# Optimization experiments

Measured on AMD Instinct MI355X. Metric: run time of the kernel, lower is better.

## Reference

```python
import jax, jax.numpy as jnp
import numpy as np

B, C, H, W = 4, 512, 64, 64
CQ = C // 8


def setup_inputs() -> dict:
    key = jax.random.key(0)
    ks = jax.random.split(key, 8)
    s_in = 1.0 / np.sqrt(C)
    return {
        "x": jax.random.normal(ks[0], (B, C, H, W), jnp.float32),
        "wq": jax.random.normal(ks[1], (CQ, C), jnp.float32) * s_in,
        "bq": jax.random.normal(ks[2], (CQ,), jnp.float32) * 0.01,
        "wk": jax.random.normal(ks[3], (CQ, C), jnp.float32) * s_in,
        "bk": jax.random.normal(ks[4], (CQ,), jnp.float32) * 0.01,
        "wv": jax.random.normal(ks[5], (C, C), jnp.float32) * s_in,
        "bv": jax.random.normal(ks[6], (C,), jnp.float32) * 0.01,
        "gamma": jax.random.normal(ks[7], (1,), jnp.float32) * 0.1,
    }


def reference(x, wq, bq, wk, bk, wv, bv, gamma):
    b, c, h, w = x.shape
    n = h * w
    xf = x.reshape(b, c, n)  # [B, C, N]; 1x1 conv == channel matmul
    q = jnp.einsum("oc,bcn->bon", wq, xf) + bq[None, :, None]  # [B, CQ, N]
    k = jnp.einsum("oc,bcn->bon", wk, xf) + bk[None, :, None]  # [B, CQ, N]
    v = jnp.einsum("oc,bcn->bon", wv, xf) + bv[None, :, None]  # [B, C, N]
    energy = jnp.einsum("bcn,bcm->bnm", q, k)  # [B, N, N]
    attn = jax.nn.softmax(energy, axis=-1)
    out = jnp.einsum("bcm,bnm->bcn", v, attn)  # [B, C, N]
    out = out.reshape(b, c, h, w)
    return gamma[0] * out + x
```

## Files before the change

kernel.cpp:

```cpp
#include <hip/hip_runtime.h>
#include <hip/hip_bf16.h>

#define BATCH 4
#define CH    512
#define NPIX  4096
#define LOG2E 1.4426950408889634f

#define BOFF  327680
#define WTOT  328320
#define PSTR  268

typedef float v4f __attribute__((ext_vector_type(4)));
typedef short v8s __attribute__((ext_vector_type(8)));
typedef unsigned short u16;

__device__ __forceinline__ float b2f(u16 v){
    union { unsigned u; float f; } x; x.u = ((unsigned)v) << 16; return x.f;
}
__device__ __forceinline__ u16 f2b(float f){
    union { float f; unsigned u; } x; x.f = f;
    unsigned r = x.u + 0x7fffu + ((x.u >> 16) & 1u);
    return (u16)(r >> 16);
}
__device__ __forceinline__ void f2b2(float a, float b, u16* o){
    union { __hip_bfloat162 v; u16 s[2]; } u;
    u.v = __float22bfloat162_rn(make_float2(a, b));
    o[0] = u.s[0]; o[1] = u.s[1];
}
__device__ __forceinline__ float fexp2(float x){
#if __has_builtin(__builtin_amdgcn_exp2f)
    return __builtin_amdgcn_exp2f(x);
#else
    return exp2f(x);
#endif
}
__device__ __forceinline__ v4f mfma16(v8s a, v8s b, v4f c){
    return __builtin_amdgcn_mfma_f32_16x16x32_bf16(a, b, c, 0, 0, 0);
}
__device__ __forceinline__ float load_s(const void* p, size_t idx, int isf32){
    return isf32 ? ((const float*)p)[idx] : b2f(((const u16*)p)[idx]);
}

__global__ void detect_kernel(const unsigned* __restrict__ x, int* __restrict__ flag){
    __shared__ int cnt;
    if (threadIdx.x == 0) cnt = 0;
    __syncthreads();
    int c = 0;
    for (int i = threadIdx.x; i < 1024; i += 64){
        unsigned e = (x[i] >> 23) & 0xFFu;
        if (e >= 64u && e < 192u) c++;
    }
    atomicAdd(&cnt, c);
    __syncthreads();
    if (threadIdx.x == 0) flag[0] = (cnt > 512) ? 1 : 0;
}

__global__ __launch_bounds__(256) void prep_kernel(
    const void* __restrict__ wq, const void* __restrict__ bq,
    const void* __restrict__ wk, const void* __restrict__ bk,
    const void* __restrict__ wv, const void* __restrict__ bv,
    u16* __restrict__ wall, const int* __restrict__ flag)
{
    const int isf32 = flag[0];
    int i = blockIdx.x * 256 + threadIdx.x;
    if (i >= WTOT) return;
    float v;
    if (i < BOFF){
        int o = i >> 9, c = i & 511;
        if (o < 64)       v = load_s(wq, (size_t)o * 512 + c, isf32);
        else if (o < 128) v = load_s(wk, (size_t)(o - 64) * 512 + c, isf32);
        else              v = load_s(wv, (size_t)(o - 128) * 512 + c, isf32);
    } else {
        int o = i - BOFF;
        if (o < 64)       v = load_s(bq, o, isf32);
        else if (o < 128) v = load_s(bk, o - 64, isf32);
        else              v = load_s(bv, o - 128, isf32);
    }
    wall[i] = f2b(v);
}

__global__ __launch_bounds__(512, 4) void proj_kernel(
    const void* __restrict__ x, const u16* __restrict__ wall,
    u16* __restrict__ Qf, u16* __restrict__ Kf, u16* __restrict__ Vf,
    u16* __restrict__ xbf, const int* __restrict__ flag)
{
    const int isf32 = flag[0];
    const int nt2 = blockIdx.x, b = blockIdx.y;
    const int n0 = nt2 * 32;
    const int t = threadIdx.x, lane = t & 63, w = t >> 6, q = lane >> 4, col = lane & 15;

    __shared__ __align__(16) u16 xT[2][32 * 72];

    const int rrow  = t >> 3;
    const int ncol4 = (t & 7) * 4;
    const size_t xbase = (size_t)b * CH * NPIX + n0 + ncol4;

    v4f acc[5][2];
    #pragma unroll
    for (int i = 0; i < 5; i++)
        #pragma unroll
        for (int j = 0; j < 2; j++) acc[i][j] = (v4f){0.f, 0.f, 0.f, 0.f};

    #define LOADX(dst_f4, cb_) do {                                          \
        const size_t src = xbase + (size_t)((cb_) * 64 + rrow) * NPIX;       \
        if (isf32) dst_f4 = *(const float4*)((const float*)x + src);         \
        else {                                                               \
            union { uint2 v; float2 f; } ldu;                                \
            ldu.v = *(const uint2*)((const u16*)x + src);                    \
            dst_f4.x = ldu.f.x; dst_f4.y = ldu.f.y; dst_f4.z = 0; dst_f4.w = 0; \
        }                                                                    \
    } while (0)

    #define CVT4(vals_, f4_) do {                                            \
        if (isf32){ f2b2(f4_.x, f4_.y, &vals_[0]); f2b2(f4_.z, f4_.w, &vals_[2]); } \
        else { union { float2 f; uint2 v; } uu; uu.f = make_float2(f4_.x, f4_.y);   \
               union { uint2 v; u16 s[4]; } ss; ss.v = uu.v;                 \
               vals_[0]=ss.s[0]; vals_[1]=ss.s[1]; vals_[2]=ss.s[2]; vals_[3]=ss.s[3]; } \
    } while (0)

    float4 g_next;
    {
        float4 g0; LOADX(g0, 0);
        u16 vals[4]; CVT4(vals, g0);
        #pragma unroll
        for (int i = 0; i < 4; i++) xT[0][(ncol4 + i) * 72 + rrow] = vals[i];
        *(uint2*)&xbf[(size_t)(b * CH + rrow) * NPIX + n0 + ncol4] = *(uint2*)vals;
        LOADX(g_next, 1);
    }
    __syncthreads();

    for (int cb = 0; cb < 8; cb++){
        const int buf = cb & 1;

        if (cb < 7){
            u16 vals[4]; CVT4(vals, g_next);
            #pragma unroll
            for (int i = 0; i < 4; i++) xT[buf ^ 1][(ncol4 + i) * 72 + rrow] = vals[i];
            *(uint2*)&xbf[(size_t)(b * CH + (cb + 1) * 64 + rrow) * NPIX + n0 + ncol4] = *(uint2*)vals;
            if (cb < 6) LOADX(g_next, cb + 2);
        }

        #pragma unroll
        for (int kh = 0; kh < 2; kh++){
            const int c0 = cb * 64 + kh * 32 + q * 8;
            v8s wf[5];
            #pragma unroll
            for (int ct = 0; ct < 5; ct++)
                wf[ct] = *(const v8s*)&wall[(size_t)(80 * w + 16 * ct + col) * 512 + c0];
            v8s a[2];
            #pragma unroll
            for (int g = 0; g < 2; g++)
                a[g] = *(const v8s*)&xT[buf][(16 * g + col) * 72 + kh * 32 + q * 8];
            #pragma unroll
            for (int ct = 0; ct < 5; ct++)
                #pragma unroll
                for (int g = 0; g < 2; g++)
                    acc[ct][g] = mfma16(a[g], wf[ct], acc[ct][g]);
        }
        __syncthreads();
    }
    #undef LOADX
    #undef CVT4

    const u16* ball = wall + BOFF;
    #pragma unroll
    for (int ct = 0; ct < 5; ct++){
        const int o = 80 * w + 16 * ct + col;
        const float bv_ = b2f(ball[o]);
        #pragma unroll
        for (int g = 0; g < 2; g++){
            const int nb = n0 + 16 * g + 4 * q;
            if (o < 64){
                const int k = o;
                size_t base = (size_t)b * NPIX * 64
                    + ((size_t)((nb >> 4) * 2 + (k >> 5))) * 512
                    + ((k & 31) >> 3) * 128 + (nb & 15) * 8 + (k & 7);
                #pragma unroll
                for (int r = 0; r < 4; r++)
                    Qf[base + r * 8] = f2b((acc[ct][g][r] + bv_) * LOG2E);
            } else if (o < 128){
                const int k = o - 64;
                size_t base = (size_t)b * NPIX * 64
                    + ((size_t)((nb >> 4) * 2 + (k >> 5))) * 512
                    + ((k & 31) >> 3) * 128 + (nb & 15) * 8 + (k & 7);
                #pragma unroll
                for (int r = 0; r < 4; r++)
                    Kf[base + r * 8] = f2b(acc[ct][g][r] + bv_);
            } else {
                const int c = o - 128;
                size_t base = (size_t)b * CH * NPIX
                    + ((size_t)((c >> 4) * 128 + (nb >> 5))) * 512
                    + ((nb & 31) >> 3) * 128 + (c & 15) * 8 + (nb & 7);
                union { uint2 u; u16 s[4]; } ov;
                #pragma unroll
                for (int r = 0; r < 4; r++)
                    ov.s[r] = f2b(acc[ct][g][r] + bv_);
                *(uint2*)&Vf[base] = ov.u;
            }
        }
    }
}

__global__ __launch_bounds__(512, 2) void attn_kernel(
    const u16* __restrict__ Qf, const u16* __restrict__ Kf, const u16* __restrict__ Vf,
    const u16* __restrict__ xbf, const void* __restrict__ gamma,
    void* __restrict__ out, const int* __restrict__ flag)
{
    const int isf32 = flag[0];
    const int bid = blockIdx.x;
    const int csplit = bid & 1;
    const int b      = (bid >> 1) & 3;
    const int ntile  = bid >> 3;
    const int n0 = ntile * 128;

    const int t = threadIdx.x, lane = t & 63, w = t >> 6, q = lane >> 4, col = lane & 15;
    const int nh = w & 1;
    const int ws = w >> 1;

    __shared__ __align__(16) u16  Plds[2][128 * PSTR];
    __shared__ __align__(16) float lsum[8][64];

    const u16* Qb = Qf + (size_t)b * NPIX * 64;
    const u16* Kb = Kf + (size_t)b * NPIX * 64;
    const u16* Vb = Vf + (size_t)b * CH * NPIX;

    v8s qa[4][2];
    #pragma unroll
    for (int g = 0; g < 4; g++)
        #pragma unroll
        for (int c2 = 0; c2 < 2; c2++)
            qa[g][c2] = *(const v8s*)&Qb[(size_t)((((n0 + 64 * nh) >> 4) + g) * 2 + c2) * 512 + lane * 8];

    float lreg[4] = {0.f, 0.f, 0.f, 0.f};

    v4f oacc[4][4];
    #pragma unroll
    for (int i = 0; i < 4; i++)
        #pragma unroll
        for (int j = 0; j < 4; j++) oacc[i][j] = (v4f){0.f, 0.f, 0.f, 0.f};

    const int ms    = 64 * ws;
    const int cslab = csplit * 256 + 64 * ws;

    for (int it = 0; it < 16; it++){
        const int m0 = it * 256;
        const int buf = it & 1;

        v8s kf[4][2];
        #pragma unroll
        for (int mt = 0; mt < 4; mt++)
            #pragma unroll
            for (int c2 = 0; c2 < 2; c2++)
                kf[mt][c2] = *(const v8s*)&Kb[(size_t)((((m0 + ms) >> 4) + mt) * 2 + c2) * 512 + lane * 8];

        #pragma unroll
        for (int g = 0; g < 4; g++){
            #pragma unroll
            for (int mt = 0; mt < 4; mt++){
                v4f sv = (v4f){-64.f, -64.f, -64.f, -64.f};
                sv = mfma16(kf[mt][0], qa[g][0], sv);
                sv = mfma16(kf[mt][1], qa[g][1], sv);
                float p0 = fexp2(sv[0]), p1 = fexp2(sv[1]);
                float p2 = fexp2(sv[2]), p3 = fexp2(sv[3]);
                lreg[g] += (p0 + p1) + (p2 + p3);
                union { uint2 u; u16 s[4]; } pk;
                f2b2(p0, p1, &pk.s[0]);
                f2b2(p2, p3, &pk.s[2]);
                *(uint2*)&Plds[buf][(64 * nh + 16 * g + col) * PSTR + ms + 16 * mt + 4 * q] = pk.u;
            }
        }

        __syncthreads();

        v8s va_c[4];
        #pragma unroll
        for (int ct = 0; ct < 4; ct++)
            va_c[ct] = *(const v8s*)&Vb[(size_t)(((cslab + 16 * ct) >> 4) * 128 + (m0 >> 5)) * 512 + lane * 8];
        #pragma unroll
        for (int kk = 0; kk < 8; kk++){
            v8s va_n[4];
            if (kk < 7){
                #pragma unroll
                for (int ct = 0; ct < 4; ct++)
                    va_n[ct] = *(const v8s*)&Vb[(size_t)(((cslab + 16 * ct) >> 4) * 128 + (m0 >> 5) + kk + 1) * 512 + lane * 8];
            }
            v8s pb[4];
            #pragma unroll
            for (int nt = 0; nt < 4; nt++)
                pb[nt] = *(const v8s*)&Plds[buf][(64 * nh + 16 * nt + col) * PSTR + 32 * kk + q * 8];
            #pragma unroll
            for (int ct = 0; ct < 4; ct++)
                #pragma unroll
                for (int nt = 0; nt < 4; nt++)
                    oacc[ct][nt] = mfma16(va_c[ct], pb[nt], oacc[ct][nt]);
            #pragma unroll
            for (int ct = 0; ct < 4; ct++) va_c[ct] = va_n[ct];
        }
    }

    #pragma unroll
    for (int g = 0; g < 4; g++){
        lreg[g] += __shfl_xor(lreg[g], 16);
        lreg[g] += __shfl_xor(lreg[g], 32);
    }
    if (lane < 16){
        #pragma unroll
        for (int g = 0; g < 4; g++)
            lsum[w][16 * g + lane] = lreg[g];
    }
    __syncthreads();

    const float gam = load_s(gamma, 0, isf32);
    float linv[4];
    #pragma unroll
    for (int nt = 0; nt < 4; nt++){
        int nn = 16 * nt + col;
        float l = lsum[nh][nn] + lsum[2 + nh][nn] + lsum[4 + nh][nn] + lsum[6 + nh][nn];
        linv[nt] = gam / l;
    }

    const size_t boff = (size_t)b * CH * NPIX;
    #pragma unroll
    for (int ct = 0; ct < 4; ct++){
        #pragma unroll
        for (int rr = 0; rr < 4; rr++){
            int c = cslab + 16 * ct + 4 * q + rr;
            size_t base = boff + (size_t)c * NPIX + n0 + 64 * nh;
            #pragma unroll
            for (int nt = 0; nt < 4; nt++){
                int n = 16 * nt + col;
                float o = oacc[ct][nt][rr] * linv[nt] + b2f(xbf[base + n]);
                if (isf32) ((float*)out)[base + n] = o;
                else       ((u16*)out)[base + n]  = f2b(o);
            }
        }
    }
}

extern "C" void kernel_launch(void* const* d_in, const int* in_sizes, int n_in,
                              void* d_out, int out_size, void* d_ws, size_t ws_size,
                              hipStream_t stream)
{
    const void* x     = d_in[0];
    const void* wq    = d_in[1];
    const void* bq    = d_in[2];
    const void* wk    = d_in[3];
    const void* bk    = d_in[4];
    const void* wv    = d_in[5];
    const void* bv    = d_in[6];
    const void* gamma = d_in[7];

    u16* Qf   = (u16*)d_ws;
    u16* Kf   = Qf + (size_t)1048576;
    u16* Vf   = Kf + (size_t)1048576;
    u16* xbf  = Vf + (size_t)8388608;
    u16* wall = xbf + (size_t)8388608;
    int* flag = (int*)(wall + WTOT + 16);

    detect_kernel<<<1, 64, 0, stream>>>((const unsigned*)x, flag);
    prep_kernel<<<(WTOT + 255) / 256, 256, 0, stream>>>(wq, bq, wk, bk, wv, bv, wall, flag);
    proj_kernel<<<dim3(128, BATCH), 512, 0, stream>>>(x, wall, Qf, Kf, Vf, xbf, flag);
    attn_kernel<<<256, 512, 0, stream>>>(Qf, Kf, Vf, xbf, gamma, d_out, flag);
}
```

Before: 254.8 us.

## Retile projection and attention kernels into smaller 256-thread blocks

The projection kernel now uses 256-thread blocks covering 64 pixels. The output channels are split across two blocks in the y dimension, and the channel reduction steps through 32-channel chunks with wider 8-element x loads. Only the first channel split writes the bf16 copy of x. The attention kernel drops the two-way pixel-half split per block, which halves its query tile and shared-memory P buffer and doubles the block count. The goal is more blocks for better occupancy and load balance, at the cost of loading x twice in projection and re-reading K/V for more query tiles in attention.

New measurement: 233.6 us. -8.3%, faster.

```diff
diff --git a/kernel.cpp b/kernel.cpp
--- a/kernel.cpp
+++ b/kernel.cpp
@@ -79,96 +79,96 @@
     wall[i] = f2b(v);
 }
 
-__global__ __launch_bounds__(512, 4) void proj_kernel(
+__global__ __launch_bounds__(256, 2) void proj_kernel(
     const void* __restrict__ x, const u16* __restrict__ wall,
     u16* __restrict__ Qf, u16* __restrict__ Kf, u16* __restrict__ Vf,
     u16* __restrict__ xbf, const int* __restrict__ flag)
 {
     const int isf32 = flag[0];
-    const int nt2 = blockIdx.x, b = blockIdx.y;
-    const int n0 = nt2 * 32;
+    const int ntile = blockIdx.x, os = blockIdx.y, b = blockIdx.z;
+    const int n0 = ntile * 64;
     const int t = threadIdx.x, lane = t & 63, w = t >> 6, q = lane >> 4, col = lane & 15;
 
-    __shared__ __align__(16) u16 xT[2][32 * 72];
+    __shared__ __align__(16) u16 xT[2][64 * 40];
 
     const int rrow  = t >> 3;
-    const int ncol4 = (t & 7) * 4;
-    const size_t xbase = (size_t)b * CH * NPIX + n0 + ncol4;
-
-    v4f acc[5][2];
+    const int ncol8 = (t & 7) * 8;
+    const size_t xbase = (size_t)b * CH * NPIX + n0 + ncol8;
+
+    v4f acc[5][4];
     #pragma unroll
     for (int i = 0; i < 5; i++)
         #pragma unroll
-        for (int j = 0; j < 2; j++) acc[i][j] = (v4f){0.f, 0.f, 0.f, 0.f};
-
-    #define LOADX(dst_f4, cb_) do {                                          \
-        const size_t src = xbase + (size_t)((cb_) * 64 + rrow) * NPIX;       \
-        if (isf32) dst_f4 = *(const float4*)((const float*)x + src);         \
-        else {                                                               \
-            union { uint2 v; float2 f; } ldu;                                \
-            ldu.v = *(const uint2*)((const u16*)x + src);                    \
-            dst_f4.x = ldu.f.x; dst_f4.y = ldu.f.y; dst_f4.z = 0; dst_f4.w = 0; \
-        }                                                                    \
+        for (int j = 0; j < 4; j++) acc[i][j] = (v4f){0.f, 0.f, 0.f, 0.f};
+
+    float4 gn0, gn1;
+
+    #define LOADX(cb_) do {                                                  \
+        const size_t src = xbase + (size_t)((cb_) * 32 + rrow) * NPIX;       \
+        if (isf32){ gn0 = *(const float4*)((const float*)x + src);           \
+                    gn1 = *(const float4*)((const float*)x + src + 4); }     \
+        else { union { uint4 v; float4 f; } lu;                              \
+               lu.v = *(const uint4*)((const u16*)x + src); gn0 = lu.f; }    \
     } while (0)
 
-    #define CVT4(vals_, f4_) do {                                            \
-        if (isf32){ f2b2(f4_.x, f4_.y, &vals_[0]); f2b2(f4_.z, f4_.w, &vals_[2]); } \
-        else { union { float2 f; uint2 v; } uu; uu.f = make_float2(f4_.x, f4_.y);   \
-               union { uint2 v; u16 s[4]; } ss; ss.v = uu.v;                 \
-               vals_[0]=ss.s[0]; vals_[1]=ss.s[1]; vals_[2]=ss.s[2]; vals_[3]=ss.s[3]; } \
+    #define CVT8(vals_) do {                                                 \
+        if (isf32){ f2b2(gn0.x, gn0.y, &vals_[0]); f2b2(gn0.z, gn0.w, &vals_[2]); \
+                    f2b2(gn1.x, gn1.y, &vals_[4]); f2b2(gn1.z, gn1.w, &vals_[6]); } \
+        else { union { float4 f; uint4 v; } uu; uu.f = gn0;                  \
+               *(uint4*)vals_ = uu.v; }                                      \
     } while (0)
 
-    float4 g_next;
     {
-        float4 g0; LOADX(g0, 0);
-        u16 vals[4]; CVT4(vals, g0);
-        #pragma unroll
-        for (int i = 0; i < 4; i++) xT[0][(ncol4 + i) * 72 + rrow] = vals[i];
-        *(uint2*)&xbf[(size_t)(b * CH + rrow) * NPIX + n0 + ncol4] = *(uint2*)vals;
-        LOADX(g_next, 1);
+        LOADX(0);
+        u16 vals[8]; CVT8(vals);
+        #pragma unroll
+        for (int i = 0; i < 8; i++) xT[0][(ncol8 + i) * 40 + rrow] = vals[i];
+        if (os == 0)
+            *(uint4*)&xbf[(size_t)(b * CH + rrow) * NPIX + n0 + ncol8] = *(uint4*)vals;
+        LOADX(1);
     }
     __syncthreads();
 
-    for (int cb = 0; cb < 8; cb++){
+    for (int cb = 0; cb < 16; cb++){
         const int buf = cb & 1;
-
-        if (cb < 7){
-            u16 vals[4]; CVT4(vals, g_next);
-            #pragma unroll
-            for (int i = 0; i < 4; i++) xT[buf ^ 1][(ncol4 + i) * 72 + rrow] = vals[i];
-            *(uint2*)&xbf[(size_t)(b * CH + (cb + 1) * 64 + rrow) * NPIX + n0 + ncol4] = *(uint2*)vals;
-            if (cb < 6) LOADX(g_next, cb + 2);
-        }
-
-        #pragma unroll
-        for (int kh = 0; kh < 2; kh++){
-            const int c0 = cb * 64 + kh * 32 + q * 8;
-            v8s wf[5];
-            #pragma unroll
-            for (int ct = 0; ct < 5; ct++)
-                wf[ct] = *(const v8s*)&wall[(size_t)(80 * w + 16 * ct + col) * 512 + c0];
-            v8s a[2];
-            #pragma unroll
-            for (int g = 0; g < 2; g++)
-                a[g] = *(const v8s*)&xT[buf][(16 * g + col) * 72 + kh * 32 + q * 8];
-            #pragma unroll
-            for (int ct = 0; ct < 5; ct++)
-                #pragma unroll
-                for (int g = 0; g < 2; g++)
-                    acc[ct][g] = mfma16(a[g], wf[ct], acc[ct][g]);
-        }
+        const int c0 = cb * 32 + q * 8;
+
+        v8s wf[5];
+        #pragma unroll
+        for (int ct = 0; ct < 5; ct++)
+            wf[ct] = *(const v8s*)&wall[(size_t)(320 * os + 80 * w + 16 * ct + col) * 512 + c0];
+
+        v8s a[4];
+        #pragma unroll
+        for (int g = 0; g < 4; g++)
+            a[g] = *(const v8s*)&xT[buf][(16 * g + col) * 40 + q * 8];
+
+        if (cb < 15){
+            u16 vals[8]; CVT8(vals);
+            #pragma unroll
+            for (int i = 0; i < 8; i++) xT[buf ^ 1][(ncol8 + i) * 40 + rrow] = vals[i];
+            if (os == 0)
+                *(uint4*)&xbf[(size_t)(b * CH + (cb + 1) * 32 + rrow) * NPIX + n0 + ncol8] = *(uint4*)vals;
+            if (cb < 14) LOADX(cb + 2);
+        }
+
+        #pragma unroll
+        for (int ct = 0; ct < 5; ct++)
+            #pragma unroll
+            for (int g = 0; g < 4; g++)
+                acc[ct][g] = mfma16(a[g], wf[ct], acc[ct][g]);
         __syncthreads();
     }
     #undef LOADX
-    #undef CVT4
+    #undef CVT8
 
     const u16* ball = wall + BOFF;
     #pragma unroll
     for (int ct = 0; ct < 5; ct++){
-        const int o = 80 * w + 16 * ct + col;
+        const int o = 320 * os + 80 * w + 16 * ct + col;
         const float bv_ = b2f(ball[o]);
         #pragma unroll
-        for (int g = 0; g < 2; g++){
+        for (int g = 0; g < 4; g++){
             const int nb = n0 + 16 * g + 4 * q;
             if (o < 64){
                 const int k = o;
@@ -201,7 +201,7 @@
     }
 }
 
-__global__ __launch_bounds__(512, 2) void attn_kernel(
+__global__ __launch_bounds__(256, 2) void attn_kernel(
     const u16* __restrict__ Qf, const u16* __restrict__ Kf, const u16* __restrict__ Vf,
     const u16* __restrict__ xbf, const void* __restrict__ gamma,
     void* __restrict__ out, const int* __restrict__ flag)
@@ -211,14 +211,12 @@
     const int csplit = bid & 1;
     const int b      = (bid >> 1) & 3;
     const int ntile  = bid >> 3;
-    const int n0 = ntile * 128;
+    const int n0 = ntile * 64;
 
     const int t = threadIdx.x, lane = t & 63, w = t >> 6, q = lane >> 4, col = lane & 15;
-    const int nh = w & 1;
-    const int ws = w >> 1;
-
-    __shared__ __align__(16) u16  Plds[2][128 * PSTR];
-    __shared__ __align__(16) float lsum[8][64];
+
+    __shared__ __align__(16) u16  Plds[2][64 * PSTR];
+    __shared__ __align__(16) float lsum[4][64];
 
     const u16* Qb = Qf + (size_t)b * NPIX * 64;
     const u16* Kb = Kf + (size_t)b * NPIX * 64;
@@ -229,7 +227,7 @@
     for (int g = 0; g < 4; g++)
         #pragma unroll
         for (int c2 = 0; c2 < 2; c2++)
-            qa[g][c2] = *(const v8s*)&Qb[(size_t)((((n0 + 64 * nh) >> 4) + g) * 2 + c2) * 512 + lane * 8];
+            qa[g][c2] = *(const v8s*)&Qb[(size_t)(((n0 >> 4) + g) * 2 + c2) * 512 + lane * 8];
 
     float lreg[4] = {0.f, 0.f, 0.f, 0.f};
 
@@ -239,8 +237,8 @@
         #pragma unroll
         for (int j = 0; j < 4; j++) oacc[i][j] = (v4f){0.f, 0.f, 0.f, 0.f};
 
-    const int ms    = 64 * ws;
-    const int cslab = csplit * 256 + 64 * ws;
+    const int ms    = 64 * w;
+    const int cslab = csplit * 256 + 64 * w;
 
     for (int it = 0; it < 16; it++){
         const int m0 = it * 256;
@@ -266,7 +264,7 @@
                 union { uint2 u; u16 s[4]; } pk;
                 f2b2(p0, p1, &pk.s[0]);
                 f2b2(p2, p3, &pk.s[2]);
-                *(uint2*)&Plds[buf][(64 * nh + 16 * g + col) * PSTR + ms + 16 * mt + 4 * q] = pk.u;
+                *(uint2*)&Plds[buf][(16 * g + col) * PSTR + ms + 16 * mt + 4 * q] = pk.u;
             }
         }
 
@@ -287,7 +285,7 @@
             v8s pb[4];
             #pragma unroll
             for (int nt = 0; nt < 4; nt++)
-                pb[nt] = *(const v8s*)&Plds[buf][(64 * nh + 16 * nt + col) * PSTR + 32 * kk + q * 8];
+                pb[nt] = *(const v8s*)&Plds[buf][(16 * nt + col) * PSTR + 32 * kk + q * 8];
             #pragma unroll
             for (int ct = 0; ct < 4; ct++)
                 #pragma unroll
@@ -315,7 +313,7 @@
     #pragma unroll
     for (int nt = 0; nt < 4; nt++){
         int nn = 16 * nt + col;
-        float l = lsum[nh][nn] + lsum[2 + nh][nn] + lsum[4 + nh][nn] + lsum[6 + nh][nn];
+        float l = lsum[0][nn] + lsum[1][nn] + lsum[2][nn] + lsum[3][nn];
         linv[nt] = gam / l;
     }
 
@@ -325,7 +323,7 @@
         #pragma unroll
         for (int rr = 0; rr < 4; rr++){
             int c = cslab + 16 * ct + 4 * q + rr;
-            size_t base = boff + (size_t)c * NPIX + n0 + 64 * nh;
+            size_t base = boff + (size_t)c * NPIX + n0;
             #pragma unroll
             for (int nt = 0; nt < 4; nt++){
                 int n = 16 * nt + col;
@@ -359,6 +357,6 @@
 
     detect_kernel<<<1, 64, 0, stream>>>((const unsigned*)x, flag);
     prep_kernel<<<(WTOT + 255) / 256, 256, 0, stream>>>(wq, bq, wk, bk, wv, bv, wall, flag);
-    proj_kernel<<<dim3(128, BATCH), 512, 0, stream>>>(x, wall, Qf, Kf, Vf, xbf, flag);
-    attn_kernel<<<256, 512, 0, stream>>>(Qf, Kf, Vf, xbf, gamma, d_out, flag);
-}
+    proj_kernel<<<dim3(64, 2, BATCH), 256, 0, stream>>>(x, wall, Qf, Kf, Vf, xbf, flag);
+    attn_kernel<<<512, 256, 0, stream>>>(Qf, Kf, Vf, xbf, gamma, d_out, flag);
+}
```
